# Kernel tuning notes

Measured on AMD Instinct MI355X. Metric: run time of the kernel, lower is better.

## Reference

```python
import jax, jax.numpy as jnp
import numpy as np
import math

SR = 16000        # sample_rate
HOP = 512         # hop_length
FMIN = 20.0
N_BINS = 84
BPO = 12          # bins_per_octave
Q = 1.0 / (2.0 ** (1.0 / BPO) - 1.0)


def setup_inputs() -> dict:
    key = jax.random.key(0)
    waveform = jax.random.normal(key, (2560000,), dtype=jnp.float32)
    return {"waveform": waveform}


def _bin_kernel(wl: int, freq: float, dtype):
    """Windowed single-DFT-bin kernel matching torch.stft row `freq_bin`.
    Returns (2,1,wl) conv kernel: [real, imag] parts of conj(e^{-2pi i f n / wl}) * hann.
    """
    n = np.arange(wl)
    # torch.hann_window default is periodic: 0.5*(1 - cos(2*pi*n/N))
    w = 0.5 - 0.5 * np.cos(2.0 * np.pi * n / wl)
    fb = min(int(freq * wl / SR), wl // 2)  # onesided stft has wl//2+1 rows
    ang = 2.0 * np.pi * fb * n / wl
    kr = (w * np.cos(ang)).astype(np.float32)
    ki = (-w * np.sin(ang)).astype(np.float32)
    return jnp.asarray(np.stack([kr, ki])[:, None, :], dtype=dtype)


def reference(waveform) -> jnp.ndarray:
    L = waveform.shape[-1]
    num_frames = (L - HOP) // HOP + 1  # matches torch code's frame count
    rows = []
    for k in range(N_BINS):
        freq = FMIN * 2.0 ** (k / BPO)
        wl = min(int(SR * Q / freq), L // 4)
        if wl < 32:  # torch code skips these bins (row stays zero)
            rows.append(jnp.zeros((num_frames,), waveform.dtype))
            continue
        pad = wl // 2  # torch.stft center=True reflect padding
        xpad = jnp.pad(waveform, (pad, pad), mode="reflect")
        kern = _bin_kernel(wl, freq, waveform.dtype)
        # strided correlation == extracting one DFT bin of every stft frame
        out = jax.lax.conv_general_dilated(
            xpad[None, None, :], kern, window_strides=(HOP,), padding="VALID"
        )[0]  # (2, n_frames_k)
        mag = jnp.sqrt(out[0] ** 2 + out[1] ** 2)
        mf = min(mag.shape[0], num_frames)
        rows.append(jnp.zeros((num_frames,), waveform.dtype).at[:mf].set(mag[:mf]))
    return jnp.stack(rows)[None]  # (1, n_bins, num_frames)
```

## Files before the change

### kernel.cpp

```cpp
#include <hip/hip_runtime.h>
#include <math.h>

#define L_IN   2560000
#define HOP    512
#define NB     84
#define NF     5000
#define PAD0   6726
#define XPLEN  2573452
#define XBLEN2 2637824
#define NTIL   80
#define SLOTS  7
#define NBLK   (NTIL*SLOTS)
#define XB_NB  1288
#define AG_NB  502

#define LDS_SZ 70656

#define XB_B 0
#define AG_B 5275648
#define P_B  7331840

typedef short bf16x8 __attribute__((ext_vector_type(8)));
typedef float f32x16 __attribute__((ext_vector_type(16)));

__device__ inline unsigned short f2bf(float f) {
  unsigned int u = __float_as_uint(f);
  return (unsigned short)((u + 0x7fffu + ((u >> 16) & 1u)) >> 16);
}

__device__ inline void load16(void* l, const void* g) {
  __builtin_amdgcn_global_load_lds((const __attribute__((address_space(1))) void*)g,
                                   (__attribute__((address_space(3))) void*)l, 16, 0, 0);
}

__global__ __launch_bounds__(256) void k_prep(const float* __restrict__ x,
                                              unsigned short* __restrict__ xb,
                                              unsigned short* __restrict__ Ag) {
  if (blockIdx.x < XB_NB) {
    int i8 = (blockIdx.x * 256 + threadIdx.x) * 8;
    bf16x8 o;
    int u0 = i8 - PAD0;
    if (u0 >= 0 && u0 + 8 <= L_IN) {
      const float2* p = (const float2*)(x + u0);
#pragma unroll
      for (int j = 0; j < 4; ++j) {
        float2 v = p[j];
        o[2 * j]     = (short)f2bf(v.x);
        o[2 * j + 1] = (short)f2bf(v.y);
      }
    } else {
#pragma unroll
      for (int j = 0; j < 8; ++j) {
        int i = i8 + j;
        float v = 0.f;
        if (i < XPLEN) {
          int u = i - PAD0;
          if (u < 0) u = -u;
          else if (u >= L_IN) u = 2 * L_IN - 2 - u;
          v = x[u];
        }
        o[j] = (short)f2bf(v);
      }
    }
    *(bf16x8*)(xb + i8) = o;
  } else {
    int g = (blockIdx.x - XB_NB) * 256 + threadIdx.x;
    int s = g >> 9, w = g & 511;
    int im = w >> 8, kk = (w >> 6) & 3, lane = w & 63;
    int mt  = (s < 211) ? 0 : ((s < 245) ? 1 : 2);
    int mst = (mt == 0) ? 0 : ((mt == 1) ? 211 : 245);
    int kst = (mt == 0) ? 0 : ((mt == 1) ? 5632 : 6528);
    int tap0 = kst + (s - mst) * 64 + kk * 16 + ((lane >> 5) << 3);
    int row = im * 32 + (lane & 31);
    int bin = mt * 32 + (row >> 1);
    bf16x8 vv;
    if (bin >= NB) {
#pragma unroll
      for (int j = 0; j < 8; ++j) vv[j] = 0;
    } else {
      double q    = 1.0 / (pow(2.0, 1.0 / 12.0) - 1.0);
      double freq = 20.0 * pow(2.0, (double)bin / 12.0);
      int wl = (int)(16000.0 * q / freq);
      if (wl > L_IN / 4) wl = L_IN / 4;
      int pad = wl >> 1;
      int fbq = (int)(freq * (double)wl / 16000.0);
      if (fbq > wl / 2) fbq = wl / 2;
      int isIm = row & 1;
      float invwl = 1.0f / (float)wl;
#pragma unroll
      for (int j = 0; j < 8; ++j) {
        int n = tap0 + j - (PAD0 - pad);
        float v = 0.f;
        if (n >= 0 && n < wl) {
          float wn = 0.5f - 0.5f * cosf(6.2831853071795865f * ((float)n * invwl));
          int m = (fbq * n) % wl;
          float a = 6.2831853071795865f * ((float)m * invwl);
          v = isIm ? (-wn * sinf(a)) : (wn * cosf(a));
        }
        vv[j] = (short)f2bf(v);
      }
    }
    *(bf16x8*)(Ag + ((size_t)s * 4096 + im * 2048 + kk * 512 + lane * 8)) = vv;
  }
}

struct AF { bf16x8 f[2][4]; };

__device__ inline void loadA(AF& a, const char* Ag, int s, int lane) {
  const char* p = Ag + ((size_t)s << 13) + lane * 16;
#pragma unroll
  for (int im = 0; im < 2; ++im)
#pragma unroll
    for (int kk = 0; kk < 4; ++kk)
      a.f[im][kk] = *(const bf16x8*)(p + im * 4096 + kk * 1024);
}

__device__ inline void readB(bf16x8 bf[4], const char* Bw, int l, int g, int lane) {
  int tb = l * 128 + ((lane >> 5) << 4);
  int ob = (g * 32 + (lane & 31)) * 1024 + tb;
#pragma unroll
  for (int kk = 0; kk < 4; ++kk) {
    int o = ob + kk * 32;
    o ^= ((o >> 10) & 15) << 4;
    bf[kk] = *(const bf16x8*)(Bw + o);
  }
}

__device__ inline void mfma8(const AF& a, const bf16x8 bf[4],
                             f32x16& accA, f32x16& accB) {
  __builtin_amdgcn_s_setprio(1);
#pragma unroll
  for (int kk = 0; kk < 4; ++kk) {
    accA = __builtin_amdgcn_mfma_f32_32x32x16_bf16(a.f[0][kk], bf[kk], accA, 0, 0, 0);
    accB = __builtin_amdgcn_mfma_f32_32x32x16_bf16(a.f[1][kk], bf[kk], accB, 0, 0, 0);
  }
  __builtin_amdgcn_s_setprio(0);
}

__global__ __launch_bounds__(256, 2) void k_gemm(const unsigned short* __restrict__ Ag,
                                                 const unsigned short* __restrict__ xb,
                                                 float* __restrict__ P,
                                                 float* __restrict__ out) {
  extern __shared__ char lds[];
  const int tid = threadIdx.x, lane = tid & 63, wv = tid >> 6;

  int bid = blockIdx.x;
  int xcd = bid & 7, loc = bid >> 3;
  int c = loc / 10, ntl = loc - c * 10;
  int nt = xcd * 10 + ntl;
  const int gs_[7] = {0, 43, 85, 127, 169, 211, 245};
  const int ns_[7] = {43, 42, 42, 42, 42, 34, 6};
  const int kb_[7] = {0, 2752, 5440, 8128, 10816, 5632, 6528};
  int gs = gs_[c], ns = ns_[c], kb = kb_[c];
  int nch = (64512 + 128 * ns + 1023) >> 10;

  const char* xsrc = (const char*)xb + (size_t)nt * 65536 + (size_t)kb * 2;
  for (int ci = wv; ci < nch; ci += 4)
    load16(lds + ci * 1024, xsrc + ci * 1024 + ((lane * 16) ^ ((ci & 15) << 4)));
  __builtin_amdgcn_sched_barrier(0);

  const char* Ab = (const char*)Ag;
  int nks = (ns - wv + 3) >> 2;
  AF a0, a1, a2;
  int s0 = gs + wv, s1 = gs + wv + 4, s2 = gs + wv + 8;
  loadA(a0, Ab, s0 > 250 ? 250 : s0, lane);
  loadA(a1, Ab, s1 > 250 ? 250 : s1, lane);
  loadA(a2, Ab, s2 > 250 ? 250 : s2, lane);

  f32x16 acc[2][2];
#pragma unroll
  for (int i = 0; i < 2; ++i)
#pragma unroll
    for (int j = 0; j < 2; ++j)
#pragma unroll
      for (int e = 0; e < 16; ++e) acc[i][j][e] = 0.f;

  asm volatile("s_waitcnt vmcnt(24)" ::: "memory");
  __syncthreads();

  bf16x8 bA[4], bB[4];
  readB(bA, lds, wv, 0, lane);

  int i = 0;
  while (i + 3 <= nks) {
    {
      int l = wv + 4 * i;
      readB(bB, lds, l, 1, lane);
      mfma8(a0, bA, acc[0][0], acc[1][0]);
      int ln = (i + 1 < nks) ? (wv + 4 * (i + 1)) : l;
      readB(bA, lds, ln, 0, lane);
      mfma8(a0, bB, acc[0][1], acc[1][1]);
      if (i + 3 < nks) loadA(a0, Ab, gs + wv + 4 * (i + 3), lane);
    }
    {
      int l = wv + 4 * (i + 1);
      readB(bB, lds, l, 1, lane);
      mfma8(a1, bA, acc[0][0], acc[1][0]);
      int ln = (i + 2 < nks) ? (wv + 4 * (i + 2)) : l;
      readB(bA, lds, ln, 0, lane);
      mfma8(a1, bB, acc[0][1], acc[1][1]);
      if (i + 4 < nks) loadA(a1, Ab, gs + wv + 4 * (i + 4), lane);
    }
    {
      int l = wv + 4 * (i + 2);
      readB(bB, lds, l, 1, lane);
      mfma8(a2, bA, acc[0][0], acc[1][0]);
      int ln = (i + 3 < nks) ? (wv + 4 * (i + 3)) : l;
      readB(bA, lds, ln, 0, lane);
      mfma8(a2, bB, acc[0][1], acc[1][1]);
      if (i + 5 < nks) loadA(a2, Ab, gs + wv + 4 * (i + 5), lane);
    }
    i += 3;
  }
  if (i < nks) {
    int l = wv + 4 * i;
    readB(bB, lds, l, 1, lane);
    mfma8(a0, bA, acc[0][0], acc[1][0]);
    int ln = (i + 1 < nks) ? (wv + 4 * (i + 1)) : l;
    readB(bA, lds, ln, 0, lane);
    mfma8(a0, bB, acc[0][1], acc[1][1]);
    if (i + 1 < nks) {
      int l1 = wv + 4 * (i + 1);
      readB(bB, lds, l1, 1, lane);
      mfma8(a1, bA, acc[0][0], acc[1][0]);
      int l2 = (i + 2 < nks) ? (wv + 4 * (i + 2)) : l1;
      readB(bA, lds, l2, 0, lane);
      mfma8(a1, bB, acc[0][1], acc[1][1]);
      if (i + 2 < nks) {
        readB(bB, lds, wv + 4 * (i + 2), 1, lane);
        mfma8(a2, bA, acc[0][0], acc[1][0]);
        mfma8(a2, bB, acc[0][1], acc[1][1]);
      }
    }
  }

  __syncthreads();
  float* Cw = (float*)(lds + wv * 16384);
#pragma unroll
  for (int im = 0; im < 2; ++im)
#pragma unroll
    for (int in_ = 0; in_ < 2; ++in_) {
      f32x16 v = acc[im][in_];
      int col = in_ * 32 + (lane & 31);
      int rb  = im * 32 + ((lane >> 5) << 2);
#pragma unroll
      for (int r = 0; r < 16; ++r) {
        int row = rb + (r & 3) + 8 * (r >> 2);
        Cw[row * 64 + col] = v[r];
      }
    }
  __syncthreads();
  const float* L0 = (const float*)lds;
  if (c < 5) {
    float* Pb = P + ((size_t)(nt * 5 + c) << 12);
#pragma unroll
    for (int e = 0; e < 16; ++e) {
      int idx = e * 256 + tid;
      Pb[idx] = L0[idx] + L0[idx + 4096] + L0[idx + 8192] + L0[idx + 12288];
    }
  } else {
    int bb = (c == 5) ? 32 : 64;
#pragma unroll
    for (int e = 0; e < 8; ++e) {
      int p = e * 256 + tid;
      int bl = p >> 6, fl = p & 63;
      int r0 = (bl * 2) * 64 + fl, r1 = r0 + 64;
      float re = L0[r0] + L0[r0 + 4096] + L0[r0 + 8192] + L0[r0 + 12288];
      float iv = L0[r1] + L0[r1 + 4096] + L0[r1 + 8192] + L0[r1 + 12288];
      int b = bb + bl, col = nt * 64 + fl;
      if (b < NB && col < NF)
        out[(size_t)b * NF + col] = sqrtf(re * re + iv * iv);
    }
  }
}

__global__ __launch_bounds__(256) void k_mag(const float* __restrict__ P,
                                             float* __restrict__ out) {
  int col = blockIdx.x * 256 + threadIdx.x;
  int b = blockIdx.y;
  if (col >= NF) return;
  int nt = col >> 6, fl = col & 63;
  const float* Pt = P + ((size_t)(nt * 5) << 12);
  float re = 0.f, iv = 0.f;
#pragma unroll
  for (int c = 0; c < 5; ++c) {
    const float* Pb = Pt + ((size_t)c << 12);
    re += Pb[(2 * b) * 64 + fl];
    iv += Pb[(2 * b + 1) * 64 + fl];
  }
  out[(size_t)b * NF + col] = sqrtf(re * re + iv * iv);
}

extern "C" void kernel_launch(void* const* d_in, const int* in_sizes, int n_in,
                              void* d_out, int out_size, void* d_ws, size_t ws_size,
                              hipStream_t stream) {
  const float* x = (const float*)d_in[0];
  char* ws = (char*)d_ws;
  unsigned short* xb = (unsigned short*)(ws + XB_B);
  unsigned short* Ag = (unsigned short*)(ws + AG_B);
  float* P           = (float*)(ws + P_B);
  float* out = (float*)d_out;

  hipFuncSetAttribute((const void*)k_gemm,
                      hipFuncAttributeMaxDynamicSharedMemorySize, LDS_SZ);

  hipLaunchKernelGGL(k_prep, dim3(XB_NB + AG_NB), dim3(256), 0, stream, x, xb, Ag);
  hipLaunchKernelGGL(k_gemm, dim3(NBLK), dim3(256), LDS_SZ, stream, Ag, xb, P, out);
  hipLaunchKernelGGL(k_mag, dim3(20, 32), dim3(256), 0, stream, P, out);
}
```

Before: 32.58 us.

## Fuse magnitude reduction into GEMM via atomic counter, precompute bin params on host

Drops the separate k_mag launch. Each k_gemm block with c<5 increments a per-tile atomic counter after writing its partial product, and the last of the five blocks sums all partials and writes the magnitudes. The per-bin double-precision pow work in k_prep is replaced by a small table computed on the host and copied asynchronously, and the accurate sinf/cosf calls become hardware revolution-based sin/cos builtins. This adds a threadfence, an atomic and a serialized reduction tail to one block per tile, plus a host-to-device copy on every call.

```diff
diff --git a/kernel.cpp b/kernel.cpp
--- a/kernel.cpp
+++ b/kernel.cpp
@@ -16,9 +16,11 @@
 
 #define LDS_SZ 70656
 
-#define XB_B 0
-#define AG_B 5275648
-#define P_B  7331840
+#define XB_B  0
+#define AG_B  5275648
+#define P_B   7331840
+#define CNT_B 13885440
+#define TB_B  13885760
 
 typedef short bf16x8 __attribute__((ext_vector_type(8)));
 typedef float f32x16 __attribute__((ext_vector_type(16)));
@@ -35,8 +37,11 @@
 
 __global__ __launch_bounds__(256) void k_prep(const float* __restrict__ x,
                                               unsigned short* __restrict__ xb,
-                                              unsigned short* __restrict__ Ag) {
+                                              unsigned short* __restrict__ Ag,
+                                              int* __restrict__ cnt,
+                                              const int* __restrict__ tb) {
   if (blockIdx.x < XB_NB) {
+    if (blockIdx.x == 0 && threadIdx.x < NTIL) cnt[threadIdx.x] = 0;
     int i8 = (blockIdx.x * 256 + threadIdx.x) * 8;
     bf16x8 o;
     int u0 = i8 - PAD0;
@@ -78,13 +83,9 @@
 #pragma unroll
       for (int j = 0; j < 8; ++j) vv[j] = 0;
     } else {
-      double q    = 1.0 / (pow(2.0, 1.0 / 12.0) - 1.0);
-      double freq = 20.0 * pow(2.0, (double)bin / 12.0);
-      int wl = (int)(16000.0 * q / freq);
-      if (wl > L_IN / 4) wl = L_IN / 4;
-      int pad = wl >> 1;
-      int fbq = (int)(freq * (double)wl / 16000.0);
-      if (fbq > wl / 2) fbq = wl / 2;
+      int wl  = tb[bin];
+      int pad = tb[NB + bin];
+      int fbq = tb[2 * NB + bin];
       int isIm = row & 1;
       float invwl = 1.0f / (float)wl;
 #pragma unroll
@@ -92,10 +93,12 @@
         int n = tap0 + j - (PAD0 - pad);
         float v = 0.f;
         if (n >= 0 && n < wl) {
-          float wn = 0.5f - 0.5f * cosf(6.2831853071795865f * ((float)n * invwl));
+          float wn = 0.5f - 0.5f * __builtin_amdgcn_cosf((float)n * invwl);
           int m = (fbq * n) % wl;
-          float a = 6.2831853071795865f * ((float)m * invwl);
-          v = isIm ? (-wn * sinf(a)) : (wn * cosf(a));
+          float rev = (float)m * invwl;
+          float cs = __builtin_amdgcn_cosf(rev);
+          float sn = __builtin_amdgcn_sinf(rev);
+          v = isIm ? (-wn * sn) : (wn * cs);
         }
         vv[j] = (short)f2bf(v);
       }
@@ -140,6 +143,7 @@
 __global__ __launch_bounds__(256, 2) void k_gemm(const unsigned short* __restrict__ Ag,
                                                  const unsigned short* __restrict__ xb,
                                                  float* __restrict__ P,
+                                                 int* __restrict__ cnt,
                                                  float* __restrict__ out) {
   extern __shared__ char lds[];
   const int tid = threadIdx.x, lane = tid & 63, wv = tid >> 6;
@@ -258,6 +262,28 @@
       int idx = e * 256 + tid;
       Pb[idx] = L0[idx] + L0[idx + 4096] + L0[idx + 8192] + L0[idx + 12288];
     }
+    __threadfence();
+    __syncthreads();
+    int* flag = (int*)(lds + 69632);
+    if (tid == 0) *flag = atomicAdd(&cnt[nt], 1);
+    __syncthreads();
+    if (*flag == 4) {
+      __threadfence();
+      const float* P0 = P + ((size_t)(nt * 5) << 12);
+#pragma unroll
+      for (int e = 0; e < 8; ++e) {
+        int p = e * 256 + tid;
+        int bl = p >> 6, fl = p & 63;
+        float re = 0.f, iv = 0.f;
+#pragma unroll
+        for (int cc = 0; cc < 5; ++cc) {
+          re += P0[cc * 4096 + (2 * bl) * 64 + fl];
+          iv += P0[cc * 4096 + (2 * bl + 1) * 64 + fl];
+        }
+        int col = nt * 64 + fl;
+        if (col < NF) out[(size_t)bl * NF + col] = sqrtf(re * re + iv * iv);
+      }
+    }
   } else {
     int bb = (c == 5) ? 32 : 64;
 #pragma unroll
@@ -274,23 +300,6 @@
   }
 }
 
-__global__ __launch_bounds__(256) void k_mag(const float* __restrict__ P,
-                                             float* __restrict__ out) {
-  int col = blockIdx.x * 256 + threadIdx.x;
-  int b = blockIdx.y;
-  if (col >= NF) return;
-  int nt = col >> 6, fl = col & 63;
-  const float* Pt = P + ((size_t)(nt * 5) << 12);
-  float re = 0.f, iv = 0.f;
-#pragma unroll
-  for (int c = 0; c < 5; ++c) {
-    const float* Pb = Pt + ((size_t)c << 12);
-    re += Pb[(2 * b) * 64 + fl];
-    iv += Pb[(2 * b + 1) * 64 + fl];
-  }
-  out[(size_t)b * NF + col] = sqrtf(re * re + iv * iv);
-}
-
 extern "C" void kernel_launch(void* const* d_in, const int* in_sizes, int n_in,
                               void* d_out, int out_size, void* d_ws, size_t ws_size,
                               hipStream_t stream) {
@@ -299,12 +308,28 @@
   unsigned short* xb = (unsigned short*)(ws + XB_B);
   unsigned short* Ag = (unsigned short*)(ws + AG_B);
   float* P           = (float*)(ws + P_B);
+  int* cnt           = (int*)(ws + CNT_B);
+  int* tbd           = (int*)(ws + TB_B);
   float* out = (float*)d_out;
+
+  static int h_tb[3 * NB];
+  {
+    double q = 1.0 / (pow(2.0, 1.0 / 12.0) - 1.0);
+    for (int b = 0; b < NB; ++b) {
+      double freq = 20.0 * pow(2.0, (double)b / 12.0);
+      int wl = (int)(16000.0 * q / freq);
+      if (wl > L_IN / 4) wl = L_IN / 4;
+      int pad = wl >> 1;
+      int fb = (int)(freq * (double)wl / 16000.0);
+      if (fb > wl / 2) fb = wl / 2;
+      h_tb[b] = wl; h_tb[NB + b] = pad; h_tb[2 * NB + b] = fb;
+    }
+  }
+  hipMemcpyAsync(tbd, h_tb, sizeof(h_tb), hipMemcpyHostToDevice, stream);
 
   hipFuncSetAttribute((const void*)k_gemm,
                       hipFuncAttributeMaxDynamicSharedMemorySize, LDS_SZ);
 
-  hipLaunchKernelGGL(k_prep, dim3(XB_NB + AG_NB), dim3(256), 0, stream, x, xb, Ag);
-  hipLaunchKernelGGL(k_gemm, dim3(NBLK), dim3(256), LDS_SZ, stream, Ag, xb, P, out);
-  hipLaunchKernelGGL(k_mag, dim3(20, 32), dim3(256), 0, stream, P, out);
-}
+  hipLaunchKernelGGL(k_prep, dim3(XB_NB + AG_NB), dim3(256), 0, stream, x, xb, Ag, cnt, tbd);
+  hipLaunchKernelGGL(k_gemm, dim3(NBLK), dim3(256), LDS_SZ, stream, Ag, xb, P, cnt, out);
+}
```

New measurement: 77.38 us. 138% more time.
